# Kernel tuning notes

Measured on AMD Instinct MI355X. Metric: run time of the kernel, lower is better.

## Reference

```python
import jax, jax.numpy as jnp
import numpy as np
from jax import lax

PAD = 1  # conv padding; with kernel 3 and stride (2,1) this preserves (D, D)


def setup_inputs() -> dict:
    key = jax.random.key(0)
    k1, k2, k3 = jax.random.split(key, 3)
    B, L, D = 16, 256, 64
    num_layer = 2
    x = jax.random.normal(k1, (B, L, D, D), dtype=jnp.float32)
    # Conv2d(in=1, out=1, kernel=3x3) per layer, stacked: (num_layer, O=1, I=1, 3, 3)
    W = jax.random.normal(k2, (num_layer, 1, 1, 3, 3), dtype=jnp.float32) * 0.1
    b = jax.random.normal(k3, (num_layer,), dtype=jnp.float32) * 0.1
    return {"x": x, "W": W, "b": b}


def _layer(x, W, b):
    # x: (B, L, D, D); W: (1, 1, 3, 3); b: scalar
    B, L, D, _ = x.shape
    xs = jnp.transpose(x, (1, 0, 2, 3))[:, :, None]  # (L, B, 1, D, D)
    h0 = jnp.zeros((B, 1, D, D), dtype=x.dtype)

    def step(h, xt):
        inp = jnp.concatenate([xt, h], axis=2)  # (B, 1, 2D, D)
        out = lax.conv_general_dilated(
            inp, W, window_strides=(2, 1),
            padding=((PAD, PAD), (PAD, PAD)),
            dimension_numbers=("NCHW", "OIHW", "NCHW"))  # (B, 1, D, D)
        h_new = jnp.tanh(out + b)
        return h_new, h_new

    _, hs = lax.scan(step, h0, xs)  # (L, B, 1, D, D)
    return jnp.transpose(hs[:, :, 0], (1, 0, 2, 3))  # (B, L, D, D)


def reference(x, W, b):
    # Stacked CnnBasedRnn layers; dropout is identity in eval mode.
    out = x
    for l in range(W.shape[0]):
        out = _layer(out, W[l], b[l])
    return out
```

## Files before the change

### kernel.cpp

```cpp
#include <hip/hip_runtime.h>
#include <math.h>

#define B_ 16
#define L_ 256
#define D_ 64

#define CHUNK 16
#define WARM  5
#define NCH   (L_ / CHUNK)
#define NTH   1024

#define PITCH 64
#define NSLOT 127
#define FBUF  (NSLOT * PITCH)
#define LDSZ  (2 * FBUF)

__device__ __forceinline__ int swz(int s) { return (s + (s >> 1)) & 7; }

__device__ __forceinline__ float ftanh(float x) {
    float ax = fabsf(x);
    float e  = __builtin_amdgcn_exp2f(-2.8853900818f * ax);
    float r  = (1.0f - e) * __builtin_amdgcn_rcpf(1.0f + e);
    return copysignf(r, x);
}

__device__ __forceinline__ float dpp_shr1(float x) {
    int r = __builtin_amdgcn_update_dpp(0, __float_as_int(x), 0x138, 0xF, 0xF, true);
    return __int_as_float(r);
}
__device__ __forceinline__ float dpp_shl1(float x) {
    int r = __builtin_amdgcn_update_dpp(0, __float_as_int(x), 0x130, 0xF, 0xF, true);
    return __int_as_float(r);
}

__global__ __launch_bounds__(NTH, 1) void fused_layer(
        const float* __restrict__ X, float* __restrict__ H,
        const float* __restrict__ Wl, const float* __restrict__ bl) {
    __shared__ float lds[LDSZ];

    const int tid    = threadIdx.x;
    const int b      = blockIdx.x >> 4;
    const int ch     = blockIdx.x & (NCH - 1);
    const int T0     = ch * CHUNK;
    const int tw     = (T0 >= WARM) ? (T0 - WARM) : 0;
    const int tend   = T0 + CHUNK;
    const int btbase = b * L_;

    const int r    = tid >> 4;
    const int l16  = tid & 15;
    const int q0   = l16;
    const int c0   = l16 << 2;
    const int rc   = (r < 63) ? r : 62;

    const int sxs = r + 1;
    const int xw  = sxs * PITCH + ((q0 ^ swz(sxs)) << 2);
    int ro[3];
#pragma unroll
    for (int ki = 0; ki < 3; ++ki) {
        const int s = 2 * rc + ki;
        ro[ki] = s * PITCH + ((q0 ^ swz(s)) << 2);
    }
    const int shh = 65 + r;
    const int hw  = shh * PITCH + ((q0 ^ swz(shh)) << 2);

    const bool le0  = (l16 == 0);
    const bool le15 = (l16 == 15);

    float w[9];
#pragma unroll
    for (int k = 0; k < 9; ++k) w[k] = Wl[k];
    const float bias = bl[0];
    const float4 z4 = make_float4(0.f, 0.f, 0.f, 0.f);

    for (int k = tid; k < LDSZ / 4; k += NTH)
        reinterpret_cast<float4*>(lds)[k] = z4;
    __syncthreads();

    float* cur = lds;
    float* nxt = lds + FBUF;

    {
        const float* xf = X + ((size_t)(btbase + tw) << 12) + (tid << 2);
        *reinterpret_cast<float4*>(cur + xw) = *reinterpret_cast<const float4*>(xf);
    }
    float4 px;
    {
        const int t1 = (tw + 1 < L_) ? tw + 1 : L_ - 1;
        const float* xf = X + ((size_t)(btbase + t1) << 12) + (tid << 2);
        px = *reinterpret_cast<const float4*>(xf);
    }
    __syncthreads();

    for (int t = tw; t < tend; ++t) {
        float4 nx;
        {
            const int t2 = (t + 2 < L_) ? t + 2 : L_ - 1;
            const float* xf = X + ((size_t)(btbase + t2) << 12) + (tid << 2);
            nx = *reinterpret_cast<const float4*>(xf);
        }

        float u0[4], u1[4], u2[4];
#pragma unroll
        for (int k = 0; k < 4; ++k) { u0[k] = 0.f; u1[k] = bias; u2[k] = 0.f; }
#pragma unroll
        for (int ki = 0; ki < 3; ++ki) {
            const float4 o4 = *reinterpret_cast<const float4*>(cur + ro[ki]);
            const float g[4] = {o4.x, o4.y, o4.z, o4.w};
            const float wa = w[ki*3], wb = w[ki*3+1], wc = w[ki*3+2];
#pragma unroll
            for (int k = 0; k < 4; ++k) {
                u0[k] = fmaf(wa, g[k], u0[k]);
                u1[k] = fmaf(wb, g[k], u1[k]);
                u2[k] = fmaf(wc, g[k], u2[k]);
            }
        }
        const float eLr = dpp_shr1(u0[3]);
        const float eRr = dpp_shl1(u2[0]);
        const float eL  = le0  ? 0.f : eLr;
        const float eR  = le15 ? 0.f : eRr;

        float o0 = ftanh(eL    + u1[0] + u2[1]);
        float o1 = ftanh(u0[0] + u1[1] + u2[2]);
        float o2 = ftanh(u0[1] + u1[2] + u2[3]);
        float o3 = ftanh(u0[2] + u1[3] + eR);

        if (r < 63 && t >= T0) {
            float* gd = H + (((size_t)(btbase + t)) << 12) + (r << 6) + c0;
            *reinterpret_cast<float4*>(gd) = make_float4(o0, o1, o2, o3);
        }
        if (r <= 61) {
            *reinterpret_cast<float4*>(nxt + hw) = make_float4(o0, o1, o2, o3);
        }
        {
            *reinterpret_cast<float4*>(nxt + xw) = px;
        }
        asm volatile("s_waitcnt lgkmcnt(0)" ::: "memory");
        __builtin_amdgcn_s_barrier();
        px = nx;
        float* tmp = cur; cur = nxt; nxt = tmp;
    }
}

#define SDEPTH 16
__global__ void scan63(float* __restrict__ dst,
                       const float* __restrict__ src,
                       const float* __restrict__ Wl,
                       const float* __restrict__ bl) {
    const int b = blockIdx.x;
    const int j = threadIdx.x;
    float w[9];
#pragma unroll
    for (int k = 0; k < 9; ++k) w[k] = Wl[k];
    const float bias = bl[0];

    const size_t ST = (size_t)D_ * D_;
    const float* s61 = src + (size_t)b * L_ * ST + 61 * 64 + j;
    const float* s62 = src + (size_t)b * L_ * ST + 62 * 64 + j;
    float*       d63 = dst + (size_t)b * L_ * ST + 63 * 64 + j;

    float s = ftanh(bias);
    d63[0] = s;

    float p61[SDEPTH], p62[SDEPTH];
#pragma unroll
    for (int u = 0; u < SDEPTH; ++u) {
        p61[u] = s61[(size_t)u * ST];
        p62[u] = s62[(size_t)u * ST];
    }

    for (int t0 = 1; t0 < 256; t0 += SDEPTH) {
#pragma unroll
        for (int u = 0; u < SDEPTH; ++u) {
            const int t = t0 + u;
            if (t > 255) break;
            const float r61 = p61[u], r62 = p62[u];
            int tp = t + SDEPTH - 1;
            if (tp > 255) tp = 255;
            p61[u] = s61[(size_t)tp * ST];
            p62[u] = s62[(size_t)tp * ST];
            float l1 = dpp_shr1(r61), q1 = dpp_shl1(r61);
            float l2 = dpp_shr1(r62), q2 = dpp_shl1(r62);
            float p = bias;
            p = fmaf(w[0], l1, p); p = fmaf(w[1], r61, p); p = fmaf(w[2], q1, p);
            p = fmaf(w[3], l2, p); p = fmaf(w[4], r62, p); p = fmaf(w[5], q2, p);
            float ls = dpp_shr1(s), rs = dpp_shl1(s);
            float z = fmaf(w[6], ls, fmaf(w[7], s, fmaf(w[8], rs, p)));
            s = ftanh(z);
            d63[(size_t)t * ST] = s;
        }
    }
}

extern "C" void kernel_launch(void* const* d_in, const int* in_sizes, int n_in,
                              void* d_out, int out_size, void* d_ws, size_t ws_size,
                              hipStream_t stream) {
    const float* x    = (const float*)d_in[0];
    const float* W    = (const float*)d_in[1];
    const float* bias = (const float*)d_in[2];
    float* out = (float*)d_out;
    float* h1  = (float*)d_ws;

    for (int l = 0; l < 2; ++l) {
        const float* X  = (l == 0) ? x  : h1;
        float*       H  = (l == 0) ? h1 : out;
        fused_layer<<<B_ * NCH, NTH, 0, stream>>>(X, H, W + l * 9, bias + l);
        scan63<<<B_, 64, 0, stream>>>(H, H, W + l * 9, bias + l);
    }
}
```

Baseline: 112.0 us.

## Read x rows directly into registers for first-level rows, shrink LDS buffer

Output rows below 32 depend only on x rows, so those threads now load their three x rows straight from global memory into registers, one timestep ahead. Only x row 63 and the hidden rows are staged through LDS, which halves the LDS footprint per buffer. This removes the LDS write and read of most of x on every step. In exchange it adds redundant global loads, since neighbouring output rows share input rows, and introduces divergent branches between row groups.

After: 104.5 us. -6.7%, faster.

```diff
diff --git a/kernel.cpp b/kernel.cpp
--- a/kernel.cpp
+++ b/kernel.cpp
@@ -11,7 +11,7 @@
 #define NTH   1024
 
 #define PITCH 64
-#define NSLOT 127
+#define NSLOT 63
 #define FBUF  (NSLOT * PITCH)
 #define LDSZ  (2 * FBUF)
 
@@ -50,18 +50,20 @@
     const int l16  = tid & 15;
     const int q0   = l16;
     const int c0   = l16 << 2;
-    const int rc   = (r < 63) ? r : 62;
-
-    const int sxs = r + 1;
-    const int xw  = sxs * PITCH + ((q0 ^ swz(sxs)) << 2);
+    const bool lvl0 = (r < 32);
+    const bool st63 = (r == 63);
+    const int  rc   = (r < 63) ? r : 62;
+
     int ro[3];
 #pragma unroll
     for (int ki = 0; ki < 3; ++ki) {
-        const int s = 2 * rc + ki;
-        ro[ki] = s * PITCH + ((q0 ^ swz(s)) << 2);
-    }
-    const int shh = 65 + r;
-    const int hw  = shh * PITCH + ((q0 ^ swz(shh)) << 2);
+        const int s = 2 * rc - 64 + ki;
+        const int sc = (s < 0) ? 0 : s;
+        ro[ki] = sc * PITCH + ((q0 ^ swz(sc)) << 2);
+    }
+    const int shh = r + 1;
+    const int hw  = (shh <= 62 ? shh : 62) * PITCH + ((q0 ^ swz(shh <= 62 ? shh : 62)) << 2);
+    const int xw  = q0 << 2;
 
     const bool le0  = (l16 == 0);
     const bool le15 = (l16 == 15);
@@ -79,24 +81,38 @@
     float* cur = lds;
     float* nxt = lds + FBUF;
 
-    {
-        const float* xf = X + ((size_t)(btbase + tw) << 12) + (tid << 2);
+    float4 cx0 = z4, cx1 = z4, cx2 = z4;
+    if (lvl0) {
+        const float* xf = X + ((size_t)(btbase + tw) << 12);
+        const int cr0 = 2 * r - 1;
+        if (cr0 >= 0) cx0 = *reinterpret_cast<const float4*>(xf + (cr0 << 6) + c0);
+        cx1 = *reinterpret_cast<const float4*>(xf + ((cr0 + 1) << 6) + c0);
+        cx2 = *reinterpret_cast<const float4*>(xf + ((cr0 + 2) << 6) + c0);
+    }
+    float4 p63 = z4;
+    if (st63) {
+        const float* xf = X + ((size_t)(btbase + tw) << 12) + (63 << 6) + c0;
         *reinterpret_cast<float4*>(cur + xw) = *reinterpret_cast<const float4*>(xf);
-    }
-    float4 px;
-    {
         const int t1 = (tw + 1 < L_) ? tw + 1 : L_ - 1;
-        const float* xf = X + ((size_t)(btbase + t1) << 12) + (tid << 2);
-        px = *reinterpret_cast<const float4*>(xf);
+        p63 = *reinterpret_cast<const float4*>(
+            X + ((size_t)(btbase + t1) << 12) + (63 << 6) + c0);
     }
     __syncthreads();
 
     for (int t = tw; t < tend; ++t) {
-        float4 nx;
-        {
+        float4 nx0 = z4, nx1 = z4, nx2 = z4, n63 = z4;
+        if (lvl0) {
+            const int tn = (t + 1 < L_) ? t + 1 : L_ - 1;
+            const float* xf = X + ((size_t)(btbase + tn) << 12);
+            const int cr0 = 2 * r - 1;
+            if (cr0 >= 0) nx0 = *reinterpret_cast<const float4*>(xf + (cr0 << 6) + c0);
+            nx1 = *reinterpret_cast<const float4*>(xf + ((cr0 + 1) << 6) + c0);
+            nx2 = *reinterpret_cast<const float4*>(xf + ((cr0 + 2) << 6) + c0);
+        }
+        if (st63) {
             const int t2 = (t + 2 < L_) ? t + 2 : L_ - 1;
-            const float* xf = X + ((size_t)(btbase + t2) << 12) + (tid << 2);
-            nx = *reinterpret_cast<const float4*>(xf);
+            n63 = *reinterpret_cast<const float4*>(
+                X + ((size_t)(btbase + t2) << 12) + (63 << 6) + c0);
         }
 
         float u0[4], u1[4], u2[4];
@@ -104,8 +120,14 @@
         for (int k = 0; k < 4; ++k) { u0[k] = 0.f; u1[k] = bias; u2[k] = 0.f; }
 #pragma unroll
         for (int ki = 0; ki < 3; ++ki) {
-            const float4 o4 = *reinterpret_cast<const float4*>(cur + ro[ki]);
-            const float g[4] = {o4.x, o4.y, o4.z, o4.w};
+            float g[4];
+            if (lvl0) {
+                const float4 o4 = (ki == 0) ? cx0 : (ki == 1) ? cx1 : cx2;
+                g[0] = o4.x; g[1] = o4.y; g[2] = o4.z; g[3] = o4.w;
+            } else {
+                const float4 o4 = *reinterpret_cast<const float4*>(cur + ro[ki]);
+                g[0] = o4.x; g[1] = o4.y; g[2] = o4.z; g[3] = o4.w;
+            }
             const float wa = w[ki*3], wb = w[ki*3+1], wc = w[ki*3+2];
 #pragma unroll
             for (int k = 0; k < 4; ++k) {
@@ -119,10 +141,10 @@
         const float eL  = le0  ? 0.f : eLr;
         const float eR  = le15 ? 0.f : eRr;
 
-        float o0 = ftanh(eL    + u1[0] + u2[1]);
-        float o1 = ftanh(u0[0] + u1[1] + u2[2]);
-        float o2 = ftanh(u0[1] + u1[2] + u2[3]);
-        float o3 = ftanh(u0[2] + u1[3] + eR);
+        const float o0 = ftanh(eL    + u1[0] + u2[1]);
+        const float o1 = ftanh(u0[0] + u1[1] + u2[2]);
+        const float o2 = ftanh(u0[1] + u1[2] + u2[3]);
+        const float o3 = ftanh(u0[2] + u1[3] + eR);
 
         if (r < 63 && t >= T0) {
             float* gd = H + (((size_t)(btbase + t)) << 12) + (r << 6) + c0;
@@ -131,12 +153,12 @@
         if (r <= 61) {
             *reinterpret_cast<float4*>(nxt + hw) = make_float4(o0, o1, o2, o3);
         }
-        {
-            *reinterpret_cast<float4*>(nxt + xw) = px;
+        if (st63) {
+            *reinterpret_cast<float4*>(nxt + xw) = p63;
         }
         asm volatile("s_waitcnt lgkmcnt(0)" ::: "memory");
         __builtin_amdgcn_s_barrier();
-        px = nx;
+        cx0 = nx0; cx1 = nx1; cx2 = nx2; p63 = n63;
         float* tmp = cur; cur = nxt; nxt = tmp;
     }
 }
```
